# Performance work log

Hardware: AMD Instinct MI355X
Metric: run time of the kernel (lower is better)

The kernel has to match this reference:

```python
import jax, jax.numpy as jnp
import numpy as np

HIDDEN = 2048
N_HEADS = 8
N_KV_HEADS = 1
HEAD_DIM = 256
ROPE_THETA = 10000.0
B, S = 2, 2048


def setup_inputs() -> dict:
    key = jax.random.key(0)
    ks = jax.random.split(key, 6)
    sc = 0.02
    hidden_states = jax.random.normal(ks[0], (B, S, HIDDEN), dtype=jnp.float32)
    position_ids = jnp.broadcast_to(jnp.arange(S, dtype=jnp.int64 if jax.config.jax_enable_x64 else jnp.int32), (B, S))
    # additive causal mask: 0 on/below diagonal, large negative above
    causal = jnp.tril(jnp.ones((S, S), dtype=bool))
    attention_mask = jnp.where(causal, 0.0, -1e9).astype(jnp.float32)[None, None, :, :]
    attention_mask = jnp.broadcast_to(attention_mask, (B, 1, S, S))
    Wq = jax.random.normal(ks[1], (HIDDEN, N_HEADS * HEAD_DIM), dtype=jnp.float32) * sc
    Wk = jax.random.normal(ks[2], (HIDDEN, N_KV_HEADS * HEAD_DIM), dtype=jnp.float32) * sc
    Wv = jax.random.normal(ks[3], (HIDDEN, N_KV_HEADS * HEAD_DIM), dtype=jnp.float32) * sc
    Wo = jax.random.normal(ks[4], (N_HEADS * HEAD_DIM, HIDDEN), dtype=jnp.float32) * sc
    return {"hidden_states": hidden_states, "position_ids": position_ids,
            "attention_mask": attention_mask, "Wq": Wq, "Wk": Wk, "Wv": Wv, "Wo": Wo}


def _rotate_half(x):
    x1, x2 = jnp.split(x, 2, axis=-1)
    return jnp.concatenate([-x2, x1], axis=-1)


def _rope_cos_sin(position_ids, dtype):
    # inv_freq: [head_dim/2]
    inv_freq = 1.0 / (ROPE_THETA ** (jnp.arange(0, HEAD_DIM, 2, dtype=jnp.float32) / HEAD_DIM))
    # freqs: [B, S, head_dim/2]
    freqs = position_ids.astype(jnp.float32)[:, :, None] * inv_freq[None, None, :]
    emb = jnp.concatenate([freqs, freqs], axis=-1)  # [B, S, head_dim]
    return jnp.cos(emb).astype(dtype), jnp.sin(emb).astype(dtype)


def reference(hidden_states, position_ids, attention_mask, Wq, Wk, Wv, Wo):
    b, s, _ = hidden_states.shape
    # projections (bias=False)
    q = (hidden_states @ Wq).reshape(b, s, N_HEADS, HEAD_DIM).transpose(0, 2, 1, 3)      # [B,H,S,D]
    k = (hidden_states @ Wk).reshape(b, s, N_KV_HEADS, HEAD_DIM).transpose(0, 2, 1, 3)   # [B,Hk,S,D]
    v = (hidden_states @ Wv).reshape(b, s, N_KV_HEADS, HEAD_DIM).transpose(0, 2, 1, 3)
    cos, sin = _rope_cos_sin(position_ids, hidden_states.dtype)  # [B,S,D]
    cos, sin = cos[:, None], sin[:, None]  # [B,1,S,D]
    q = q * cos + _rotate_half(q) * sin
    k = k * cos + _rotate_half(k) * sin
    # repeat_kv for GQA
    n_rep = N_HEADS // N_KV_HEADS
    k = jnp.repeat(k, n_rep, axis=1)  # [B,H,S,D]
    v = jnp.repeat(v, n_rep, axis=1)
    scale = HEAD_DIM ** -0.5
    scores = jnp.einsum('bhqd,bhkd->bhqk', q, k) * scale + attention_mask
    attn_weights = jax.nn.softmax(scores.astype(jnp.float32), axis=-1).astype(q.dtype)
    attn_out = jnp.einsum('bhqk,bhkd->bhqd', attn_weights, v)
    attn_out = attn_out.transpose(0, 2, 1, 3).reshape(b, s, N_HEADS * HEAD_DIM)
    out = attn_out @ Wo
    return out, attn_weights
```

## Files before the change

### kernel.cpp

```cpp
#include <hip/hip_runtime.h>
#include <hip/hip_bf16.h>
#include <math.h>

typedef __attribute__((ext_vector_type(4))) float f32x4;
typedef __attribute__((ext_vector_type(8))) __bf16 bf16x8;
typedef __attribute__((ext_vector_type(8))) unsigned short u16x8;

#define HID    2048
#define NHEADS 8
#define HDIM   256
#define SEQ    2048
#define BATCH  2
#define ROWS   (BATCH*SEQ)
#define QKVN   (NHEADS*HDIM + 2*HDIM)
#define NBH    (BATCH*NHEADS)

typedef __attribute__((address_space(1))) const void gvoid_t;
typedef __attribute__((address_space(3))) void lvoid_t;

__device__ __forceinline__ void gload16(const void* g, void* l){
  __builtin_amdgcn_global_load_lds((gvoid_t*)g, (lvoid_t*)l, 16, 0, 0);
}

__device__ __forceinline__ float bf2f(unsigned short u){
  union { unsigned int i; float f; } x; x.i = ((unsigned int)u) << 16; return x.f;
}
__device__ __forceinline__ unsigned short f2bf(float f){
  union { float f; unsigned int i; } x; x.f = f;
  unsigned int u = x.i;
  return (unsigned short)((u + 0x7FFFu + ((u >> 16) & 1u)) >> 16);
}

__global__ __launch_bounds__(256)
void k_prep(const float* __restrict__ hs, unsigned short* __restrict__ hsb,
            const float* __restrict__ Wq, const float* __restrict__ Wk,
            const float* __restrict__ Wv, const float* __restrict__ Wo,
            unsigned short* __restrict__ wqkvT, unsigned short* __restrict__ woT){
  int bid = (int)blockIdx.x;
  if (bid < 2048){
    long i = ((long)bid * 256 + threadIdx.x) * 16;
    f32x4 x0 = *(const f32x4*)(hs + i);
    f32x4 x1 = *(const f32x4*)(hs + i + 4);
    f32x4 x2 = *(const f32x4*)(hs + i + 8);
    f32x4 x3 = *(const f32x4*)(hs + i + 12);
    u16x8 w0, w1;
    #pragma unroll
    for (int j = 0; j < 4; ++j){
      w0[j]   = f2bf(x0[j]);
      w0[4+j] = f2bf(x1[j]);
      w1[j]   = f2bf(x2[j]);
      w1[4+j] = f2bf(x3[j]);
    }
    *(u16x8*)(hsb + i)     = w0;
    *(u16x8*)(hsb + i + 8) = w1;
    return;
  }
  __shared__ float t[32][33];
  bid -= 2048;
  const float* src; unsigned short* dst; int srcCols, gx, local;
  if (bid < 4096)      { src = Wq; dst = wqkvT;                        srcCols = HID;  gx = 64; local = bid; }
  else if (bid < 4608) { src = Wk; dst = wqkvT + (long)HID*HID;        srcCols = HDIM; gx = 8;  local = bid - 4096; }
  else if (bid < 5120) { src = Wv; dst = wqkvT + (long)(HID+HDIM)*HID; srcCols = HDIM; gx = 8;  local = bid - 4608; }
  else                 { src = Wo; dst = woT;                          srcCols = HID;  gx = 64; local = bid - 5120; }
  int bx = (local % gx) * 32;
  int by = (local / gx) * 32;
  int tx = threadIdx.x & 31, ty = threadIdx.x >> 5;
  #pragma unroll
  for (int i = 0; i < 4; ++i){
    int rr = ty + i*8;
    t[rr][tx] = src[(long)(by + rr)*srcCols + bx + tx];
  }
  __syncthreads();
  #pragma unroll
  for (int i = 0; i < 4; ++i){
    int rr = ty + i*8;
    dst[(long)(bx + rr)*HID + by + tx] = f2bf(t[tx][rr]);
  }
}

__global__ __launch_bounds__(256)
void k_mid(const unsigned short* __restrict__ qkv, const int* __restrict__ pos_ids,
           unsigned short* __restrict__ Qb, unsigned short* __restrict__ Kb,
           unsigned short* __restrict__ VT){
  int bid = (int)blockIdx.x;
  int tid = threadIdx.x;
  if (bid < ROWS){
    int row = bid;
    float pos = (float)pos_ids[row];
    const unsigned short* r = qkv + (long)row * QKVN;
    #pragma unroll
    for (int it = 0; it < 4; ++it){
      int p = it*256 + tid;
      int d = p & 127, h = p >> 7;
      int col = h*HDIM + d;
      float inv = exp2f((float)d * -0.10381025296523132f);
      float ang = pos * inv;
      float sn, cs; sincosf(ang, &sn, &cs);
      float x0 = bf2f(r[col]), x1 = bf2f(r[col + 128]);
      Qb[(long)row*HID + col]       = f2bf(x0*cs - x1*sn);
      Qb[(long)row*HID + col + 128] = f2bf(x1*cs + x0*sn);
    }
    if (tid < 128){
      int d = tid;
      float inv = exp2f((float)d * -0.10381025296523132f);
      float ang = pos * inv;
      float sn, cs; sincosf(ang, &sn, &cs);
      float x0 = bf2f(r[HID + d]), x1 = bf2f(r[HID + d + 128]);
      Kb[(long)row*HDIM + d]       = f2bf(x0*cs - x1*sn);
      Kb[(long)row*HDIM + d + 128] = f2bf(x1*cs + x0*sn);
    }
    return;
  }
  __shared__ unsigned short t[32][34];
  int local = bid - ROWS;
  int b  = local >> 9;
  int rem = local & 511;
  int s0 = (rem >> 3) * 32;
  int d0 = (rem & 7) * 32;
  int tx = tid & 31, ty = tid >> 5;
  #pragma unroll
  for (int i = 0; i < 4; ++i){
    int rr = ty + i*8;
    t[rr][tx] = qkv[(long)(b*SEQ + s0 + rr)*QKVN + HID + HDIM + d0 + tx];
  }
  __syncthreads();
  #pragma unroll
  for (int i = 0; i < 4; ++i){
    int dd = ty + i*8;
    VT[((long)b*HDIM + d0 + dd)*SEQ + s0 + tx] = t[tx][dd];
  }
}

__global__ __launch_bounds__(512, 4)
void k_fused(const unsigned short* __restrict__ Qb, const unsigned short* __restrict__ Kb,
             const unsigned short* __restrict__ VT, float* __restrict__ S,
             unsigned short* __restrict__ AOb){
  int bh = blockIdx.x, b = bh >> 3, h = bh & 7;
  int y = (int)blockIdx.y;
  int ss = (y < 16) ? (31 - y) : (y - 16);
  int qbase = ss * 64;
  int T = 2 * (ss + 1);

  float* Sh = S + (long)bh * SEQ * SEQ;
  const unsigned short* Qh = Qb + (long)b*SEQ*HID + (long)h*HDIM;
  const unsigned short* Kh = Kb + (long)b*SEQ*HDIM;
  const unsigned short* Vh = VT + (long)b*HDIM*SEQ;

  __shared__ unsigned short lK[2][32*256];
  __shared__ __bf16 lA[2][64*40];
  __shared__ float lWl[8][64];
  __shared__ float mli[64];

  int tid = threadIdx.x, lane = tid & 63, w = tid >> 6;
  int wr = w >> 1, wc = w & 1;

#define STAGE_K(kt_, buf_)                                                      \
  { _Pragma("unroll")                                                           \
    for (int t = 0; t < 2; ++t){                                                \
      int seg = w*2 + t;                                                        \
      int row = seg*2 + (lane >> 5);                                            \
      int cb  = ((lane & 31)*16) ^ ((row & 7) << 4);                            \
      gload16(Kh + (long)((kt_)*32 + row)*HDIM + (cb >> 1),                     \
              (char*)lK[buf_] + seg*1024);                                      \
    } }

#define QKT(buf_)                                                               \
  { _Pragma("unroll")                                                           \
    for (int kk = 0; kk < 8; ++kk){                                             \
      int rk = wc*16 + (lane & 15);                                             \
      bf16x8 bk = *(const bf16x8*)((const char*)lK[buf_] + rk*512 +             \
                   ((kk*64 + (lane >> 4)*16) ^ ((rk & 7) << 4)));               \
      accs = __builtin_amdgcn_mfma_f32_16x16x32_bf16(aq[kk], bk, accs, 0, 0, 0);\
    } }

  bf16x8 aq[8];
  {
    const unsigned short* qrow = Qh + (long)(qbase + wr*16 + (lane & 15))*HID + (lane >> 4)*8;
    #pragma unroll
    for (int kk = 0; kk < 8; ++kk)
      aq[kk] = *(const bf16x8*)(qrow + kk*32);
  }

  f32x4 accs;
  f32x4 acc_o[4][2];
  float oL[4];
  #pragma unroll
  for (int q = 0; q < 4; ++q){ accs[q] = 0.f; oL[q] = 0.f; }
  #pragma unroll
  for (int m = 0; m < 4; ++m)
    #pragma unroll
    for (int n = 0; n < 2; ++n)
      #pragma unroll
      for (int q = 0; q < 4; ++q) acc_o[m][n][q] = 0.f;

  STAGE_K(0, 0)
  STAGE_K(1, 1)
  asm volatile("s_waitcnt vmcnt(2)" ::: "memory");
  __builtin_amdgcn_s_barrier();
  for (int kt = 0; kt < T; ++kt){
    __builtin_amdgcn_s_setprio(1);
    QKT(kt & 1)
    __builtin_amdgcn_s_setprio(0);
    if (kt*32 + wc*16 + 15 <= qbase + wr*16){
      #pragma unroll
      for (int ri = 0; ri < 4; ++ri){
        int rowl = wr*16 + (lane >> 4)*4 + ri;
        int coll = wc*16 + (lane & 15);
        float e = __expf(accs[ri]*0.0625f - 8.0f);
        oL[ri] += e;
        lA[kt & 1][rowl*40 + coll] = (__bf16)e;
        accs[ri] = 0.f;
      }
    } else {
      #pragma unroll
      for (int ri = 0; ri < 4; ++ri){
        int rowl = wr*16 + (lane >> 4)*4 + ri;
        int coll = wc*16 + (lane & 15);
        float e = (kt*32 + coll <= qbase + rowl) ? __expf(accs[ri]*0.0625f - 8.0f) : 0.f;
        oL[ri] += e;
        lA[kt & 1][rowl*40 + coll] = (__bf16)e;
        accs[ri] = 0.f;
      }
    }
    bf16x8 vf0 = *(const bf16x8*)(Vh + (long)(w*32 +      (lane & 15))*SEQ + kt*32 + (lane >> 4)*8);
    bf16x8 vf1 = *(const bf16x8*)(Vh + (long)(w*32 + 16 + (lane & 15))*SEQ + kt*32 + (lane >> 4)*8);
    asm volatile("s_waitcnt lgkmcnt(0)" ::: "memory");
    asm volatile("s_waitcnt vmcnt(2)" ::: "memory");
    __builtin_amdgcn_s_barrier();
    if (kt + 2 < T) STAGE_K(kt + 2, kt & 1)
    __builtin_amdgcn_s_setprio(1);
    #pragma unroll
    for (int m2 = 0; m2 < 4; ++m2){
      int rq = m2*16 + (lane & 15);
      bf16x8 ap = *(const bf16x8*)&lA[kt & 1][rq*40 + (lane >> 4)*8];
      acc_o[m2][0] = __builtin_amdgcn_mfma_f32_16x16x32_bf16(ap, vf0, acc_o[m2][0], 0, 0, 0);
      acc_o[m2][1] = __builtin_amdgcn_mfma_f32_16x16x32_bf16(ap, vf1, acc_o[m2][1], 0, 0, 0);
    }
    __builtin_amdgcn_s_setprio(0);
  }

  #pragma unroll
  for (int ri = 0; ri < 4; ++ri){
    float v = oL[ri];
    #pragma unroll
    for (int off = 1; off < 16; off <<= 1) v += __shfl_xor(v, off);
    if ((lane & 15) == 0)
      lWl[w][wr*16 + (lane >> 4)*4 + ri] = v;
  }
  __syncthreads();
  if (tid < 64){
    int g = (tid >> 4) * 2;
    mli[tid] = 1.0f / (lWl[g][tid] + lWl[g+1][tid]);
  }
  __syncthreads();

  float ils[4];
  #pragma unroll
  for (int ri = 0; ri < 4; ++ri)
    ils[ri] = mli[wr*16 + (lane >> 4)*4 + ri];

  #pragma unroll
  for (int m2 = 0; m2 < 4; ++m2){
    #pragma unroll
    for (int ri = 0; ri < 4; ++ri){
      int row = m2*16 + (lane >> 4)*4 + ri;
      float il = mli[row];
      long gr = (long)b*SEQ + qbase + row;
      #pragma unroll
      for (int n = 0; n < 2; ++n){
        int col = w*32 + n*16 + (lane & 15);
        AOb[gr*HID + h*HDIM + col] = f2bf(acc_o[m2][n][ri] * il);
      }
    }
  }

  STAGE_K(0, 0)
  STAGE_K(1, 1)
  asm volatile("s_waitcnt vmcnt(2)" ::: "memory");
  __builtin_amdgcn_s_barrier();
  for (int kt = 0; kt < T; ++kt){
    __builtin_amdgcn_s_setprio(1);
    QKT(kt & 1)
    __builtin_amdgcn_s_setprio(0);
    if (kt*32 + wc*16 + 15 <= qbase + wr*16){
      #pragma unroll
      for (int ri = 0; ri < 4; ++ri){
        int rowl = wr*16 + (lane >> 4)*4 + ri;
        int coll = wc*16 + (lane & 15);
        Sh[(long)(qbase + rowl)*SEQ + kt*32 + coll] =
            __expf(accs[ri]*0.0625f - 8.0f) * ils[ri];
        accs[ri] = 0.f;
      }
    } else {
      #pragma unroll
      for (int ri = 0; ri < 4; ++ri){
        int rowl = wr*16 + (lane >> 4)*4 + ri;
        int coll = wc*16 + (lane & 15);
        float p = (kt*32 + coll <= qbase + rowl)
                  ? __expf(accs[ri]*0.0625f - 8.0f) * ils[ri] : 0.f;
        Sh[(long)(qbase + rowl)*SEQ + kt*32 + coll] = p;
        accs[ri] = 0.f;
      }
    }
    asm volatile("s_waitcnt vmcnt(4)" ::: "memory");
    __builtin_amdgcn_s_barrier();
    if (kt + 2 < T) STAGE_K(kt + 2, kt & 1)
  }

  {
    f32x4 z4; z4[0]=0.f; z4[1]=0.f; z4[2]=0.f; z4[3]=0.f;
    int row = qbase + (tid >> 3);
    for (int c = T*32 + (tid & 7)*4; c < SEQ; c += 32)
      *(f32x4*)&Sh[(long)row*SEQ + c] = z4;
  }
#undef STAGE_K
#undef QKT
}

template<int OUTF32>
__global__ __launch_bounds__(512, 1)
void gemm256(const unsigned short* __restrict__ A16, const unsigned short* __restrict__ BT,
             void* __restrict__ Cv, int lda, int ldb, int ldc, int K){
  constexpr int BM = 256, BN = 128, BK = 64;
  int m0 = blockIdx.x * BM, n0 = blockIdx.y * BN;

  __shared__ unsigned short lA[2][BM*BK];
  __shared__ unsigned short lB[2][BN*BK];

  int tid = threadIdx.x, lane = tid & 63, w = tid >> 6;
  int wr = w >> 1, wc = w & 1;
  int srow = lane >> 3;
  int vswz = ((lane & 7) ^ ((lane >> 3) & 7)) * 8;

  f32x4 acc[4][4];
  #pragma unroll
  for (int m = 0; m < 4; ++m)
    #pragma unroll
    for (int n = 0; n < 4; ++n)
      #pragma unroll
      for (int q = 0; q < 4; ++q) acc[m][n][q] = 0.f;

  int NT = K / BK;

#define STAGE256(kt_, buf_)                                                    \
  { int k0_ = (kt_) * BK;                                                      \
    _Pragma("unroll")                                                          \
    for (int t = 0; t < 4; ++t){                                               \
      int seg = w*4 + t;                                                       \
      const unsigned short* src = A16 + (long)(m0 + seg*8 + srow)*lda + k0_ + vswz; \
      gload16(src, (char*)lA[buf_] + seg*1024);                                \
    }                                                                          \
    _Pragma("unroll")                                                          \
    for (int t = 0; t < 2; ++t){                                               \
      int seg = w*2 + t;                                                       \
      const unsigned short* src = BT + (long)(n0 + seg*8 + srow)*ldb + k0_ + vswz; \
      gload16(src, (char*)lB[buf_] + seg*1024);                                \
    } }

  STAGE256(0, 0)
  STAGE256(1, 1)
  int cur = 0;

  for (int kt = 0; kt < NT; ++kt){
    if (kt < NT - 1) asm volatile("s_waitcnt vmcnt(6)" ::: "memory");
    else             asm volatile("s_waitcnt vmcnt(0)" ::: "memory");
    __builtin_amdgcn_s_barrier();

    const char* La = (const char*)lA[cur];
    const char* Lb = (const char*)lB[cur];
    __builtin_amdgcn_s_setprio(1);
    #pragma unroll
    for (int kk = 0; kk < 2; ++kk){
      bf16x8 af[4], bfr[4];
      #pragma unroll
      for (int m = 0; m < 4; ++m){
        int row = wr*64 + m*16 + (lane & 15);
        int kb = (kk*64 + (lane >> 4)*16) ^ ((row & 7) << 4);
        af[m] = *(const bf16x8*)(La + row*128 + kb);
      }
      #pragma unroll
      for (int n = 0; n < 4; ++n){
        int row = wc*64 + n*16 + (lane & 15);
        int kb = (kk*64 + (lane >> 4)*16) ^ ((row & 7) << 4);
        bfr[n] = *(const bf16x8*)(Lb + row*128 + kb);
      }
      #pragma unroll
      for (int m = 0; m < 4; ++m)
        #pragma unroll
        for (int n = 0; n < 4; ++n)
          acc[m][n] = __builtin_amdgcn_mfma_f32_16x16x32_bf16(af[m], bfr[n], acc[m][n], 0, 0, 0);
    }
    __builtin_amdgcn_s_setprio(0);
    __builtin_amdgcn_s_barrier();
    if (kt + 2 < NT) STAGE256(kt + 2, cur)
    cur ^= 1;
  }
#undef STAGE256

  #pragma unroll
  for (int m = 0; m < 4; ++m){
    #pragma unroll
    for (int ri = 0; ri < 4; ++ri){
      int orow = m0 + wr*64 + m*16 + (lane >> 4)*4 + ri;
      #pragma unroll
      for (int n = 0; n < 4; ++n){
        int ocol = n0 + wc*64 + n*16 + (lane & 15);
        float vv = acc[m][n][ri];
        if (OUTF32) ((float*)Cv)[(long)orow*ldc + ocol] = vv;
        else        ((unsigned short*)Cv)[(long)orow*ldc + ocol] = f2bf(vv);
      }
    }
  }
}

extern "C" void kernel_launch(void* const* d_in, const int* in_sizes, int n_in,
                              void* d_out, int out_size, void* d_ws, size_t ws_size,
                              hipStream_t stream){
  const float* hs  = (const float*)d_in[0];
  const int*   pos = (const int*)  d_in[1];
  const float* Wq  = (const float*)d_in[3];
  const float* Wk  = (const float*)d_in[4];
  const float* Wv  = (const float*)d_in[5];
  const float* Wo  = (const float*)d_in[6];

  float* out  = (float*)d_out;
  float* Sbuf = out + (long)ROWS * HID;

  unsigned short* wsp   = (unsigned short*)d_ws;
  unsigned short* hsb   = wsp;
  unsigned short* wqkvT = hsb   + (long)ROWS*HID;
  unsigned short* woT   = wqkvT + (long)QKVN*HID;
  unsigned short* qkvb  = woT   + (long)HID*HID;
  unsigned short* Qb    = qkvb  + (long)ROWS*QKVN;
  unsigned short* Kb    = Qb    + (long)ROWS*HID;
  unsigned short* VT    = Kb    + (long)ROWS*HDIM;
  unsigned short* AOb   = VT    + (long)BATCH*HDIM*SEQ;

  k_prep<<<2048 + 9216, 256, 0, stream>>>(hs, hsb, Wq, Wk, Wv, Wo, wqkvT, woT);

  gemm256<0><<<dim3(ROWS/256, QKVN/128), 512, 0, stream>>>(
      hsb, wqkvT, qkvb, HID, HID, QKVN, HID);

  k_mid<<<ROWS + 1024, 256, 0, stream>>>(qkvb, pos, Qb, Kb, VT);

  k_fused<<<dim3(NBH, 32), 512, 0, stream>>>(Qb, Kb, VT, Sbuf, AOb);

  gemm256<1><<<dim3(ROWS/256, HID/128), 512, 0, stream>>>(
      AOb, woT, out, HID, HID, HID, HID);
}
```

Before: 302.7 us.

## Replace second QK^T pass with bf16 scratch stash and separate normalize kernel

The fused attention kernel used to recompute QK^T and exp in a second pass to write normalized fp32 probabilities. It now writes the unnormalized bf16 exponentials into the front half of each output row during the first pass, along with per-row inverse sums. A new k_norm kernel reads those values back, scales them, and writes the full fp32 rows including the masked zeros. This removes the duplicated matmul and exp work at the cost of an extra kernel launch, extra read/write traffic on the 128MB score buffer, and a reduced attention result precision of bf16.

```diff
diff --git a/kernel.cpp b/kernel.cpp
--- a/kernel.cpp
+++ b/kernel.cpp
@@ -134,7 +134,7 @@
 __global__ __launch_bounds__(512, 4)
 void k_fused(const unsigned short* __restrict__ Qb, const unsigned short* __restrict__ Kb,
              const unsigned short* __restrict__ VT, float* __restrict__ S,
-             unsigned short* __restrict__ AOb){
+             unsigned short* __restrict__ AOb, float* __restrict__ mlg){
   int bh = blockIdx.x, b = bh >> 3, h = bh & 7;
   int y = (int)blockIdx.y;
   int ss = (y < 16) ? (31 - y) : (y - 16);
@@ -208,7 +208,9 @@
         int coll = wc*16 + (lane & 15);
         float e = __expf(accs[ri]*0.0625f - 8.0f);
         oL[ri] += e;
-        lA[kt & 1][rowl*40 + coll] = (__bf16)e;
+        unsigned short eb = f2bf(e);
+        lA[kt & 1][rowl*40 + coll] = *(__bf16*)&eb;
+        ((unsigned short*)&Sh[(long)(qbase + rowl)*SEQ])[kt*32 + coll] = eb;
         accs[ri] = 0.f;
       }
     } else {
@@ -218,14 +220,16 @@
         int coll = wc*16 + (lane & 15);
         float e = (kt*32 + coll <= qbase + rowl) ? __expf(accs[ri]*0.0625f - 8.0f) : 0.f;
         oL[ri] += e;
-        lA[kt & 1][rowl*40 + coll] = (__bf16)e;
+        unsigned short eb = f2bf(e);
+        lA[kt & 1][rowl*40 + coll] = *(__bf16*)&eb;
+        ((unsigned short*)&Sh[(long)(qbase + rowl)*SEQ])[kt*32 + coll] = eb;
         accs[ri] = 0.f;
       }
     }
     bf16x8 vf0 = *(const bf16x8*)(Vh + (long)(w*32 +      (lane & 15))*SEQ + kt*32 + (lane >> 4)*8);
     bf16x8 vf1 = *(const bf16x8*)(Vh + (long)(w*32 + 16 + (lane & 15))*SEQ + kt*32 + (lane >> 4)*8);
     asm volatile("s_waitcnt lgkmcnt(0)" ::: "memory");
-    asm volatile("s_waitcnt vmcnt(2)" ::: "memory");
+    asm volatile("s_waitcnt vmcnt(6)" ::: "memory");
     __builtin_amdgcn_s_barrier();
     if (kt + 2 < T) STAGE_K(kt + 2, kt & 1)
     __builtin_amdgcn_s_setprio(1);
@@ -250,14 +254,11 @@
   __syncthreads();
   if (tid < 64){
     int g = (tid >> 4) * 2;
-    mli[tid] = 1.0f / (lWl[g][tid] + lWl[g+1][tid]);
+    float vv = 1.0f / (lWl[g][tid] + lWl[g+1][tid]);
+    mli[tid] = vv;
+    mlg[(long)bh*SEQ + qbase + tid] = vv;
   }
   __syncthreads();
-
-  float ils[4];
-  #pragma unroll
-  for (int ri = 0; ri < 4; ++ri)
-    ils[ri] = mli[wr*16 + (lane >> 4)*4 + ri];
 
   #pragma unroll
   for (int m2 = 0; m2 < 4; ++m2){
@@ -273,48 +274,47 @@
       }
     }
   }
-
-  STAGE_K(0, 0)
-  STAGE_K(1, 1)
-  asm volatile("s_waitcnt vmcnt(2)" ::: "memory");
-  __builtin_amdgcn_s_barrier();
-  for (int kt = 0; kt < T; ++kt){
-    __builtin_amdgcn_s_setprio(1);
-    QKT(kt & 1)
-    __builtin_amdgcn_s_setprio(0);
-    if (kt*32 + wc*16 + 15 <= qbase + wr*16){
-      #pragma unroll
-      for (int ri = 0; ri < 4; ++ri){
-        int rowl = wr*16 + (lane >> 4)*4 + ri;
-        int coll = wc*16 + (lane & 15);
-        Sh[(long)(qbase + rowl)*SEQ + kt*32 + coll] =
-            __expf(accs[ri]*0.0625f - 8.0f) * ils[ri];
-        accs[ri] = 0.f;
-      }
-    } else {
-      #pragma unroll
-      for (int ri = 0; ri < 4; ++ri){
-        int rowl = wr*16 + (lane >> 4)*4 + ri;
-        int coll = wc*16 + (lane & 15);
-        float p = (kt*32 + coll <= qbase + rowl)
-                  ? __expf(accs[ri]*0.0625f - 8.0f) * ils[ri] : 0.f;
-        Sh[(long)(qbase + rowl)*SEQ + kt*32 + coll] = p;
-        accs[ri] = 0.f;
-      }
-    }
-    asm volatile("s_waitcnt vmcnt(4)" ::: "memory");
-    __builtin_amdgcn_s_barrier();
-    if (kt + 2 < T) STAGE_K(kt + 2, kt & 1)
-  }
-
-  {
-    f32x4 z4; z4[0]=0.f; z4[1]=0.f; z4[2]=0.f; z4[3]=0.f;
-    int row = qbase + (tid >> 3);
-    for (int c = T*32 + (tid & 7)*4; c < SEQ; c += 32)
-      *(f32x4*)&Sh[(long)row*SEQ + c] = z4;
-  }
 #undef STAGE_K
 #undef QKT
+}
+
+__global__ __launch_bounds__(512)
+void k_norm(float* __restrict__ S, const float* __restrict__ mlg){
+  int g = (int)blockIdx.x * 8 + (int)(threadIdx.x >> 6);
+  int lane = threadIdx.x & 63;
+  int bh = g >> 11, srow = g & (SEQ - 1);
+  float il = mlg[g];
+  float* row = S + (long)bh*SEQ*SEQ + (long)srow*SEQ;
+  const unsigned short* pk = (const unsigned short*)row;
+
+  int c0 = lane*16, c1 = lane*16 + 1024;
+  bool v0 = (c0 <= srow), v1 = (c1 <= srow);
+  u16x8 e0a, e0b, e1a, e1b;
+  if (v0){ e0a = *(const u16x8*)(pk + c0);   e0b = *(const u16x8*)(pk + c0 + 8); }
+  if (v1){ e1a = *(const u16x8*)(pk + c1);   e1b = *(const u16x8*)(pk + c1 + 8); }
+  asm volatile("s_waitcnt vmcnt(0)" ::: "memory");
+
+  f32x4 o[4];
+  #pragma unroll
+  for (int q = 0; q < 4; ++q)
+    #pragma unroll
+    for (int j = 0; j < 4; ++j){
+      int k = q*4 + j;
+      unsigned short eb = v0 ? ((k < 8) ? e0a[k] : e0b[k-8]) : (unsigned short)0;
+      o[q][j] = (c0 + k <= srow) ? bf2f(eb) * il : 0.f;
+    }
+  #pragma unroll
+  for (int q = 0; q < 4; ++q) *(f32x4*)(row + c0 + q*4) = o[q];
+  #pragma unroll
+  for (int q = 0; q < 4; ++q)
+    #pragma unroll
+    for (int j = 0; j < 4; ++j){
+      int k = q*4 + j;
+      unsigned short eb = v1 ? ((k < 8) ? e1a[k] : e1b[k-8]) : (unsigned short)0;
+      o[q][j] = (c1 + k <= srow) ? bf2f(eb) * il : 0.f;
+    }
+  #pragma unroll
+  for (int q = 0; q < 4; ++q) *(f32x4*)(row + c1 + q*4) = o[q];
 }
 
 template<int OUTF32>
@@ -436,6 +436,8 @@
   unsigned short* VT    = Kb    + (long)ROWS*HDIM;
   unsigned short* AOb   = VT    + (long)BATCH*HDIM*SEQ;
 
+  float* mlg = (float*)hsb;
+
   k_prep<<<2048 + 9216, 256, 0, stream>>>(hs, hsb, Wq, Wk, Wv, Wo, wqkvT, woT);
 
   gemm256<0><<<dim3(ROWS/256, QKVN/128), 512, 0, stream>>>(
@@ -443,7 +445,9 @@
 
   k_mid<<<ROWS + 1024, 256, 0, stream>>>(qkvb, pos, Qb, Kb, VT);
 
-  k_fused<<<dim3(NBH, 32), 512, 0, stream>>>(Qb, Kb, VT, Sbuf, AOb);
+  k_fused<<<dim3(NBH, 32), 512, 0, stream>>>(Qb, Kb, VT, Sbuf, AOb, mlg);
+
+  k_norm<<<(NBH*SEQ)/8, 512, 0, stream>>>(Sbuf, mlg);
 
   gemm256<1><<<dim3(ROWS/256, HID/128), 512, 0, stream>>>(
       AOb, woT, out, HID, HID, HID, HID);
```

Result: slower. 361.8 us (+19.5%).
